# Performance work log

Hardware: AMD Instinct MI355X
Metric: run time of the kernel (lower is better)

Reference implementation:

```python
import jax, jax.numpy as jnp
import numpy as np

B, T, D, H = 8, 512, 1024, 16
DH = D // H  # per-head feature dim (64)


def setup_inputs() -> dict:
    key = jax.random.key(0)
    ks = jax.random.split(key, 10)
    s = 1.0 / np.sqrt(DH)
    inp = {
        "X_data": jax.random.normal(ks[0], (B, T, D), dtype=jnp.float32),
        "mask": jnp.ones((B, T), dtype=jnp.int32),
        # per-head Q/K/V projections (each SelfAttention has its own d_h x d_h weights)
        "Wq": jax.random.normal(ks[1], (H, DH, DH), dtype=jnp.float32) * s,
        "bq": jnp.zeros((H, DH), dtype=jnp.float32),
        "Wk": jax.random.normal(ks[2], (H, DH, DH), dtype=jnp.float32) * s,
        "bk": jnp.zeros((H, DH), dtype=jnp.float32),
        "Wv": jax.random.normal(ks[3], (H, DH, DH), dtype=jnp.float32) * s,
        "bv": jnp.zeros((H, DH), dtype=jnp.float32),
        # AttentionFusion: linear on concatenated head outputs -> len_feature_new
        "Wf": jax.random.normal(ks[4], (D, D), dtype=jnp.float32) * (1.0 / np.sqrt(D)),
        "bf": jnp.zeros((D,), dtype=jnp.float32),
    }
    return inp


def reference(X_data, mask, Wq, bq, Wk, bk, Wv, bv, Wf, bf):
    # Split features into heads: [B, T, H, DH] (equal partitions since D % H == 0)
    Xh = X_data.reshape(B, T, H, DH)
    # Batched per-head projections (replaces the Python loop over heads)
    Q = jnp.einsum("bthd,hde->bhte", Xh, Wq) + bq[None, :, None, :]
    K = jnp.einsum("bthd,hde->bhte", Xh, Wk) + bk[None, :, None, :]
    V = jnp.einsum("bthd,hde->bhte", Xh, Wv) + bv[None, :, None, :]
    scale = 1.0 / jnp.sqrt(jnp.asarray(DH, dtype=Q.dtype))
    scores = jnp.einsum("bhqe,bhke->bhqk", Q, K) * scale  # [B, H, T, T]
    scores = jnp.where(mask[:, None, None, :] > 0, scores, jnp.asarray(-1e9, scores.dtype))
    att = jax.nn.softmax(scores, axis=-1)
    out = jnp.einsum("bhqk,bhke->bhqe", att, V)  # [B, H, T, DH]
    # Concatenate heads (same order as the per-head loop) and fuse
    out = out.transpose(0, 2, 1, 3).reshape(B, T, D)
    fused = out @ Wf + bf  # AttentionFusion linear
    return fused
```

## Files before the change

kernel.cpp:

```cpp
#include <hip/hip_runtime.h>
#include <math.h>

#define B 8
#define T 512
#define D 1024
#define H 16
#define DH 64

typedef __bf16 bf16;
typedef __attribute__((ext_vector_type(8))) __bf16 bf16x8;
typedef __attribute__((ext_vector_type(4))) __bf16 bf16x4;
typedef __attribute__((ext_vector_type(4))) float f32x4;

__device__ __forceinline__ void gld16(const void* g, void* l) {
    __builtin_amdgcn_global_load_lds(
        (const __attribute__((address_space(1))) void*)g,
        (__attribute__((address_space(3))) void*)l, 16, 0, 0);
}


#define EXP2SCALE 1.44269504088896f

__global__ __launch_bounds__(256, 2) void qkv_attn(
    const float* __restrict__ X, const int* __restrict__ mask,
    const float* __restrict__ Wq, const float* __restrict__ Wk,
    const float* __restrict__ Wv,
    const float* __restrict__ bq, const float* __restrict__ bv,
    const float* __restrict__ Wf, bf16* __restrict__ WfT,
    bf16* __restrict__ Ob)
{
    __shared__ __align__(16) char smem[80384];

    if (blockIdx.x >= 512) {
        bf16* Ts = (bf16*)smem;
        const int ti = blockIdx.x - 512, tid = threadIdx.x;
        const int k0 = (ti >> 4) * 64, n0 = (ti & 15) * 64;
        for (int i = tid; i < 1024; i += 256) {
            const int k = i >> 4, nq = (i & 15) * 4;
            const float4 w = *(const float4*)(Wf + (size_t)(k0 + k) * D + n0 + nq);
            Ts[(nq + 0) * 72 + k] = (bf16)w.x; Ts[(nq + 1) * 72 + k] = (bf16)w.y;
            Ts[(nq + 2) * 72 + k] = (bf16)w.z; Ts[(nq + 3) * 72 + k] = (bf16)w.w;
        }
        __syncthreads();
        for (int i = tid; i < 512; i += 256) {
            const int n = i >> 3, kc = (i & 7) * 8;
            *(bf16x8*)(WfT + (size_t)(n0 + n) * D + k0 + kc) = *(const bf16x8*)&Ts[n * 72 + kc];
        }
        return;
    }

    bf16* Wks = (bf16*)(smem);
    bf16* Wvs = (bf16*)(smem + 8192);
    bf16* Pl  = (bf16*)(smem + 53248);
    bf16* Xkt = (bf16*)(smem + 71680);
    int*  msk = (int*)(smem + 79872);
    bf16* Wqs   = (bf16*)(smem + 16384);
    bf16* Xq    = Pl;
    bf16* Stage = Pl;
    bf16* Ostage = Pl;

    const int bh = blockIdx.x & 127, q0 = (blockIdx.x >> 7) * 128;
    const int b = bh >> 4, h = bh & 15;
    const int tid = threadIdx.x, wave = tid >> 6, lane = tid & 63;
    const int quad = lane >> 4, l15 = lane & 15;

    const int pkrow = wave * 16 + (lane >> 2);
    const int pc0 = (lane & 3) * 2;

    float bqr[4], bvr[4];
#pragma unroll
    for (int nt = 0; nt < 4; ++nt) {
        bqr[nt] = bq[h * DH + nt * 16 + l15];
        bvr[nt] = bv[h * DH + nt * 16 + l15];
    }

    float4 px0, px1, px2, px3;
    {
        const float* src = X + (size_t)(b * T + pkrow) * D + h * DH + pc0 * 8;
        px0 = *(const float4*)src; px1 = *(const float4*)(src + 4);
        px2 = *(const float4*)(src + 8); px3 = *(const float4*)(src + 12);
    }
    int mreg = (tid < 64) ? mask[(size_t)b * T + tid] : 0;

    for (int i = tid; i < 1024; i += 256) {
        const int d = i >> 4, eq4 = (i & 15) * 4;
        const int cw = ((d >> 3)) * 8 + (d & 7);
        const float4 wq4 = *(const float4*)(Wq + (size_t)h * 4096 + d * 64 + eq4);
        const float4 wk4 = *(const float4*)(Wk + (size_t)h * 4096 + d * 64 + eq4);
        const float4 wv4 = *(const float4*)(Wv + (size_t)h * 4096 + d * 64 + eq4);
#pragma unroll
        for (int j = 0; j < 4; ++j) {
            const int e = eq4 + j;
            const int idx = e * 64 + (((d >> 3) ^ (e & 7)) * 8) + (d & 7);
            Wqs[idx] = (bf16)((const float*)&wq4)[j];
            Wks[idx] = (bf16)((const float*)&wk4)[j];
            Wvs[idx] = (bf16)((const float*)&wv4)[j];
        }
        (void)cw;
    }
    for (int i = tid; i < 1024; i += 256) {
        const int row = i >> 3, c = i & 7;
        const float* src = X + (size_t)(b * T + q0 + row) * D + h * DH + c * 8;
        const float4 x0 = *(const float4*)src;
        const float4 x1 = *(const float4*)(src + 4);
        bf16x8 t;
        t[0] = (bf16)x0.x; t[1] = (bf16)x0.y; t[2] = (bf16)x0.z; t[3] = (bf16)x0.w;
        t[4] = (bf16)x1.x; t[5] = (bf16)x1.y; t[6] = (bf16)x1.z; t[7] = (bf16)x1.w;
        *(bf16x8*)&Xq[row * 64 + ((c ^ (row & 7)) * 8)] = t;
    }
    __syncthreads();

    {
        f32x4 accQ[2][4] = {};
#pragma unroll
        for (int ks = 0; ks < 2; ++ks) {
            bf16x8 af[2], bfr[4];
#pragma unroll
            for (int mt = 0; mt < 2; ++mt) {
                const int row = wave * 32 + mt * 16 + l15;
                af[mt] = *(const bf16x8*)&Xq[row * 64 + (((ks * 4 + quad) ^ (l15 & 7)) * 8)];
            }
#pragma unroll
            for (int nt = 0; nt < 4; ++nt)
                bfr[nt] = *(const bf16x8*)&Wqs[(nt * 16 + l15) * 64 + (((ks * 4 + quad) ^ (l15 & 7)) * 8)];
#pragma unroll
            for (int mt = 0; mt < 2; ++mt)
#pragma unroll
                for (int nt = 0; nt < 4; ++nt)
                    accQ[mt][nt] = __builtin_amdgcn_mfma_f32_16x16x32_bf16(af[mt], bfr[nt], accQ[mt][nt], 0, 0, 0);
        }
        __syncthreads();
        const float qs = 0.125f * EXP2SCALE;
#pragma unroll
        for (int mt = 0; mt < 2; ++mt)
#pragma unroll
            for (int nt = 0; nt < 4; ++nt)
#pragma unroll
                for (int reg = 0; reg < 4; ++reg)
                    Stage[(wave * 32 + mt * 16 + quad * 4 + reg) * 72 + nt * 16 + l15] =
                        (bf16)((accQ[mt][nt][reg] + bqr[nt]) * qs);
        __builtin_amdgcn_wave_barrier();
    }
    bf16x8 qf[2][2];
#pragma unroll
    for (int mt = 0; mt < 2; ++mt)
#pragma unroll
        for (int ks = 0; ks < 2; ++ks)
            qf[mt][ks] = *(const bf16x8*)&Stage[(wave * 32 + mt * 16 + l15) * 72 + ks * 32 + quad * 8];

    f32x4 acc[2][4] = {};
    float lst2[2] = {0.f, 0.f};

    for (int kt = 0; kt < 8; ++kt) {
        const int p = kt & 1;
        bf16* Ks  = (bf16*)(smem + 16384 + p * 9216);
        bf16* Vts = (bf16*)(smem + 34816 + p * 9216);

        {
            bf16x8 t0, t1;
            t0[0] = (bf16)px0.x; t0[1] = (bf16)px0.y; t0[2] = (bf16)px0.z; t0[3] = (bf16)px0.w;
            t0[4] = (bf16)px1.x; t0[5] = (bf16)px1.y; t0[6] = (bf16)px1.z; t0[7] = (bf16)px1.w;
            t1[0] = (bf16)px2.x; t1[1] = (bf16)px2.y; t1[2] = (bf16)px2.z; t1[3] = (bf16)px2.w;
            t1[4] = (bf16)px3.x; t1[5] = (bf16)px3.y; t1[6] = (bf16)px3.z; t1[7] = (bf16)px3.w;
            *(bf16x8*)&Xkt[pkrow * 64 + ((pc0 ^ (pkrow & 7)) * 8)] = t0;
            *(bf16x8*)&Xkt[pkrow * 64 + (((pc0 + 1) ^ (pkrow & 7)) * 8)] = t1;
            if (tid < 64) msk[p * 64 + tid] = mreg;
        }
        __builtin_amdgcn_wave_barrier();

        if (kt < 7) {
            const float* src = X + (size_t)(b * T + (kt + 1) * 64 + pkrow) * D + h * DH + pc0 * 8;
            px0 = *(const float4*)src; px1 = *(const float4*)(src + 4);
            px2 = *(const float4*)(src + 8); px3 = *(const float4*)(src + 12);
            if (tid < 64) mreg = mask[(size_t)b * T + (kt + 1) * 64 + tid];
        }

        {
            bf16x8 afkv[2];
#pragma unroll
            for (int ks = 0; ks < 2; ++ks)
                afkv[ks] = *(const bf16x8*)&Xkt[(wave * 16 + l15) * 64 + (((ks * 4 + quad) ^ (l15 & 7)) * 8)];
            f32x4 accK[4] = {}, accV[4] = {};
#pragma unroll
            for (int ks = 0; ks < 2; ++ks)
#pragma unroll
                for (int nt = 0; nt < 4; ++nt) {
                    const bf16x8 bk8 = *(const bf16x8*)&Wks[(nt * 16 + l15) * 64 + (((ks * 4 + quad) ^ (l15 & 7)) * 8)];
                    accK[nt] = __builtin_amdgcn_mfma_f32_16x16x32_bf16(bk8, afkv[ks], accK[nt], 0, 0, 0);
                    const bf16x8 bv8 = *(const bf16x8*)&Wvs[(nt * 16 + l15) * 64 + (((ks * 4 + quad) ^ (l15 & 7)) * 8)];
                    accV[nt] = __builtin_amdgcn_mfma_f32_16x16x32_bf16(afkv[ks], bv8, accV[nt], 0, 0, 0);
                }
#pragma unroll
            for (int nt = 0; nt < 4; ++nt) {
                bf16x4 kp;
#pragma unroll
                for (int reg = 0; reg < 4; ++reg) kp[reg] = (bf16)accK[nt][reg];
                *(bf16x4*)&Ks[(wave * 16 + l15) * 72 + nt * 16 + quad * 4] = kp;
                bf16x4 vp;
#pragma unroll
                for (int reg = 0; reg < 4; ++reg) vp[reg] = (bf16)accV[nt][reg];
                *(bf16x4*)&Vts[(nt * 16 + l15) * 72 + wave * 16 + quad * 4] = vp;
            }
        }
        __syncthreads();

        bf16* Plw = Pl + wave * (32 * 72);
        {
            bf16x8 kf[4][2];
#pragma unroll
            for (int nt = 0; nt < 4; ++nt)
#pragma unroll
                for (int ks = 0; ks < 2; ++ks)
                    kf[nt][ks] = *(const bf16x8*)&Ks[(nt * 16 + l15) * 72 + ks * 32 + quad * 8];
            int4 mv4[4];
#pragma unroll
            for (int nt = 0; nt < 4; ++nt)
                mv4[nt] = *(const int4*)&msk[p * 64 + nt * 16 + quad * 4];
#pragma unroll
            for (int mt = 0; mt < 2; ++mt) {
                f32x4 s[4] = {};
#pragma unroll
                for (int ks = 0; ks < 2; ++ks)
#pragma unroll
                    for (int nt = 0; nt < 4; ++nt)
                        s[nt] = __builtin_amdgcn_mfma_f32_16x16x32_bf16(kf[nt][ks], qf[mt][ks], s[nt], 0, 0, 0);
#pragma unroll
                for (int nt = 0; nt < 4; ++nt) {
                    bf16x4 pp;
                    const float p0 = (mv4[nt].x > 0) ? exp2f(s[nt][0]) : 0.f;
                    const float p1 = (mv4[nt].y > 0) ? exp2f(s[nt][1]) : 0.f;
                    const float p2 = (mv4[nt].z > 0) ? exp2f(s[nt][2]) : 0.f;
                    const float p3 = (mv4[nt].w > 0) ? exp2f(s[nt][3]) : 0.f;
                    lst2[mt] += (p0 + p1) + (p2 + p3);
                    pp[0] = (bf16)p0; pp[1] = (bf16)p1; pp[2] = (bf16)p2; pp[3] = (bf16)p3;
                    *(bf16x4*)&Plw[(mt * 16 + l15) * 72 + nt * 16 + quad * 4] = pp;
                }
            }
        }
        __builtin_amdgcn_wave_barrier();

#pragma unroll
        for (int kc = 0; kc < 2; ++kc) {
            const bf16x8 pf0 = *(const bf16x8*)&Plw[(l15) * 72 + kc * 32 + quad * 8];
            const bf16x8 pf1 = *(const bf16x8*)&Plw[(16 + l15) * 72 + kc * 32 + quad * 8];
#pragma unroll
            for (int nt = 0; nt < 4; ++nt) {
                const bf16x8 vf = *(const bf16x8*)&Vts[(nt * 16 + l15) * 72 + kc * 32 + quad * 8];
                acc[0][nt] = __builtin_amdgcn_mfma_f32_16x16x32_bf16(pf0, vf, acc[0][nt], 0, 0, 0);
                acc[1][nt] = __builtin_amdgcn_mfma_f32_16x16x32_bf16(pf1, vf, acc[1][nt], 0, 0, 0);
            }
        }
    }

    __builtin_amdgcn_wave_barrier();
    float inv_r[2][4];
#pragma unroll
    for (int mt = 0; mt < 2; ++mt) {
        float l = lst2[mt];
        l += __shfl_xor(l, 16);
        l += __shfl_xor(l, 32);
        const float inv = 1.f / l;
#pragma unroll
        for (int reg = 0; reg < 4; ++reg)
            inv_r[mt][reg] = __shfl(inv, (lane & 48) | (quad * 4 + reg));
    }
#pragma unroll
    for (int mt = 0; mt < 2; ++mt)
#pragma unroll
        for (int reg = 0; reg < 4; ++reg) {
            const int row = wave * 32 + mt * 16 + quad * 4 + reg;
#pragma unroll
            for (int nt = 0; nt < 4; ++nt)
                Ostage[row * 72 + nt * 16 + l15] =
                    (bf16)(acc[mt][nt][reg] * inv_r[mt][reg] + bvr[nt]);
        }
    __syncthreads();
    for (int i = tid; i < 1024; i += 256) {
        const int row = i >> 3, c = (i & 7) * 8;
        *(bf16x8*)(Ob + ((size_t)b * T + q0 + row) * D + h * DH + c) =
            *(const bf16x8*)&Ostage[row * 72 + c];
    }
}

__global__ __launch_bounds__(256, 2) void fuse_mfma(
    const bf16* __restrict__ Ob, const bf16* __restrict__ WfT,
    const float* __restrict__ bfv, float* __restrict__ out)
{
    __shared__ __align__(16) char smem[65536];

    const int col0 = blockIdx.x * 128;
    const int row0 = blockIdx.y * 128;
    const int tid = threadIdx.x, wave = tid >> 6, lane = tid & 63;
    const int quad = lane >> 4, l15 = lane & 15;
    const int lr = lane >> 3, lc = lane & 7;
    const int wm = wave * 32;

    f32x4 acc[2][8] = {};

    auto stage = [&](int k0, int buf) {
        bf16* As = (bf16*)(smem + buf * 16384);
        bf16* Bs = (bf16*)(smem + 32768 + buf * 16384);
#pragma unroll
        for (int j = 0; j < 4; ++j) {
            const int row = wm + j * 8 + lr;
            gld16(Ob + (size_t)(row0 + row) * D + k0 + ((lc ^ (row & 7)) * 8),
                  &As[(wm + j * 8) * 64]);
            gld16(WfT + (size_t)(col0 + row) * D + k0 + ((lc ^ (row & 7)) * 8),
                  &Bs[(wm + j * 8) * 64]);
        }
    };

    stage(0, 0);
    __syncthreads();

    for (int i = 0; i < 16; ++i) {
        const int buf = i & 1;
        if (i < 15) stage((i + 1) * 64, buf ^ 1);
        bf16* As = (bf16*)(smem + buf * 16384);
        bf16* Bs = (bf16*)(smem + 32768 + buf * 16384);
#pragma unroll
        for (int ks = 0; ks < 2; ++ks) {
            bf16x8 af[2], bfr[8];
#pragma unroll
            for (int mt = 0; mt < 2; ++mt) {
                const int row = wm + mt * 16 + l15;
                af[mt] = *(const bf16x8*)&As[row * 64 + (((ks * 4 + quad) ^ (l15 & 7)) * 8)];
            }
#pragma unroll
            for (int nt = 0; nt < 8; ++nt)
                bfr[nt] = *(const bf16x8*)&Bs[(nt * 16 + l15) * 64 + (((ks * 4 + quad) ^ (l15 & 7)) * 8)];
#pragma unroll
            for (int mt = 0; mt < 2; ++mt)
#pragma unroll
                for (int nt = 0; nt < 8; ++nt)
                    acc[mt][nt] = __builtin_amdgcn_mfma_f32_16x16x32_bf16(af[mt], bfr[nt], acc[mt][nt], 0, 0, 0);
        }
        __syncthreads();
    }

    float* Ofs = (float*)smem;
    float bias[8];
#pragma unroll
    for (int nt = 0; nt < 8; ++nt) bias[nt] = bfv[col0 + nt * 16 + l15];
#pragma unroll
    for (int cp = 0; cp < 2; ++cp) {
        if (cp) __syncthreads();
#pragma unroll
        for (int mt = 0; mt < 2; ++mt)
#pragma unroll
            for (int reg = 0; reg < 4; ++reg) {
                const int row = wm + mt * 16 + quad * 4 + reg;
#pragma unroll
                for (int nn = 0; nn < 4; ++nn)
                    Ofs[row * 68 + nn * 16 + l15] = acc[mt][cp * 4 + nn][reg] + bias[cp * 4 + nn];
            }
        __syncthreads();
        for (int i = tid; i < 2048; i += 256) {
            const int row = i >> 4, c = (i & 15) * 4;
            *(float4*)(out + (size_t)(row0 + row) * D + col0 + cp * 64 + c) =
                *(const float4*)&Ofs[row * 68 + c];
        }
    }
}

extern "C" void kernel_launch(void* const* d_in, const int* in_sizes, int n_in,
                              void* d_out, int out_size, void* d_ws, size_t ws_size,
                              hipStream_t stream) {
    const float* X   = (const float*)d_in[0];
    const int* mask  = (const int*)d_in[1];
    const float* Wq  = (const float*)d_in[2];
    const float* bq  = (const float*)d_in[3];
    const float* Wk  = (const float*)d_in[4];
    const float* bk  = (const float*)d_in[5];
    const float* Wv  = (const float*)d_in[6];
    const float* bv  = (const float*)d_in[7];
    const float* Wf  = (const float*)d_in[8];
    const float* bfv = (const float*)d_in[9];
    float* out = (float*)d_out;
    (void)bk;

    bf16* wsb = (bf16*)d_ws;
    const size_t QN = (size_t)B * H * T * DH;
    bf16* Ob  = wsb;
    bf16* WfT = wsb + QN;

    qkv_attn<<<dim3(768), 256, 0, stream>>>(X, mask, Wq, Wk, Wv, bq, bv, Wf, WfT, Ob);
    fuse_mfma<<<dim3(D / 128, (B * T) / 128), 256, 0, stream>>>(Ob, WfT, bfv, out);
}
```

Measured before the change: 126.0 us.

## Fuse attention and output projection into one kernel with flag-based inter-block sync

```diff
diff --git a/kernel.cpp b/kernel.cpp
--- a/kernel.cpp
+++ b/kernel.cpp
@@ -20,33 +20,43 @@
 
 
 #define EXP2SCALE 1.44269504088896f
-
-__global__ __launch_bounds__(256, 2) void qkv_attn(
+#define MAGIC 0x5AD0C0DEu
+
+__global__ __launch_bounds__(256, 2) void fused_all(
     const float* __restrict__ X, const int* __restrict__ mask,
     const float* __restrict__ Wq, const float* __restrict__ Wk,
     const float* __restrict__ Wv,
     const float* __restrict__ bq, const float* __restrict__ bv,
     const float* __restrict__ Wf, bf16* __restrict__ WfT,
-    bf16* __restrict__ Ob)
+    bf16* __restrict__ Ob,
+    unsigned int* __restrict__ obF, unsigned int* __restrict__ wfF,
+    const float* __restrict__ bfv, float* __restrict__ out)
 {
     __shared__ __align__(16) char smem[80384];
 
-    if (blockIdx.x >= 512) {
+    const int bid = blockIdx.x, tid = threadIdx.x;
+    const int wave = tid >> 6, lane = tid & 63;
+    const int quad = lane >> 4, l15 = lane & 15;
+    const int lr = lane >> 3, lc = lane & 7;
+
+    {
         bf16* Ts = (bf16*)smem;
-        const int ti = blockIdx.x - 512, tid = threadIdx.x;
-        const int k0 = (ti >> 4) * 64, n0 = (ti & 15) * 64;
-        for (int i = tid; i < 1024; i += 256) {
-            const int k = i >> 4, nq = (i & 15) * 4;
+        const int tj = bid >> 1, half = bid & 1;
+        const int k0 = (tj >> 4) * 64, n0 = (tj & 15) * 64 + half * 32;
+        for (int i = tid; i < 512; i += 256) {
+            const int k = i >> 3, nq = (i & 7) * 4;
             const float4 w = *(const float4*)(Wf + (size_t)(k0 + k) * D + n0 + nq);
             Ts[(nq + 0) * 72 + k] = (bf16)w.x; Ts[(nq + 1) * 72 + k] = (bf16)w.y;
             Ts[(nq + 2) * 72 + k] = (bf16)w.z; Ts[(nq + 3) * 72 + k] = (bf16)w.w;
         }
         __syncthreads();
-        for (int i = tid; i < 512; i += 256) {
+        for (int i = tid; i < 256; i += 256) {
             const int n = i >> 3, kc = (i & 7) * 8;
             *(bf16x8*)(WfT + (size_t)(n0 + n) * D + k0 + kc) = *(const bf16x8*)&Ts[n * 72 + kc];
         }
-        return;
+        __syncthreads();
+        if (tid == 0)
+            __hip_atomic_store(&wfF[bid], MAGIC, __ATOMIC_RELEASE, __HIP_MEMORY_SCOPE_AGENT);
     }
 
     bf16* Wks = (bf16*)(smem);
@@ -59,10 +69,8 @@
     bf16* Stage = Pl;
     bf16* Ostage = Pl;
 
-    const int bh = blockIdx.x & 127, q0 = (blockIdx.x >> 7) * 128;
+    const int bh = bid & 127, q0 = (bid >> 7) * 128;
     const int b = bh >> 4, h = bh & 15;
-    const int tid = threadIdx.x, wave = tid >> 6, lane = tid & 63;
-    const int quad = lane >> 4, l15 = lane & 15;
 
     const int pkrow = wave * 16 + (lane >> 2);
     const int pc0 = (lane & 3) * 2;
@@ -84,7 +92,6 @@
 
     for (int i = tid; i < 1024; i += 256) {
         const int d = i >> 4, eq4 = (i & 15) * 4;
-        const int cw = ((d >> 3)) * 8 + (d & 7);
         const float4 wq4 = *(const float4*)(Wq + (size_t)h * 4096 + d * 64 + eq4);
         const float4 wk4 = *(const float4*)(Wk + (size_t)h * 4096 + d * 64 + eq4);
         const float4 wv4 = *(const float4*)(Wv + (size_t)h * 4096 + d * 64 + eq4);
@@ -96,7 +103,6 @@
             Wks[idx] = (bf16)((const float*)&wk4)[j];
             Wvs[idx] = (bf16)((const float*)&wv4)[j];
         }
-        (void)cw;
     }
     for (int i = tid; i < 1024; i += 256) {
         const int row = i >> 3, c = i & 7;
@@ -280,85 +286,93 @@
         *(bf16x8*)(Ob + ((size_t)b * T + q0 + row) * D + h * DH + c) =
             *(const bf16x8*)&Ostage[row * 72 + c];
     }
-}
-
-__global__ __launch_bounds__(256, 2) void fuse_mfma(
-    const bf16* __restrict__ Ob, const bf16* __restrict__ WfT,
-    const float* __restrict__ bfv, float* __restrict__ out)
-{
-    __shared__ __align__(16) char smem[65536];
-
-    const int col0 = blockIdx.x * 128;
-    const int row0 = blockIdx.y * 128;
-    const int tid = threadIdx.x, wave = tid >> 6, lane = tid & 63;
-    const int quad = lane >> 4, l15 = lane & 15;
-    const int lr = lane >> 3, lc = lane & 7;
-    const int wm = wave * 32;
-
-    f32x4 acc[2][8] = {};
-
-    auto stage = [&](int k0, int buf) {
-        bf16* As = (bf16*)(smem + buf * 16384);
-        bf16* Bs = (bf16*)(smem + 32768 + buf * 16384);
-#pragma unroll
-        for (int j = 0; j < 4; ++j) {
-            const int row = wm + j * 8 + lr;
-            gld16(Ob + (size_t)(row0 + row) * D + k0 + ((lc ^ (row & 7)) * 8),
-                  &As[(wm + j * 8) * 64]);
-            gld16(WfT + (size_t)(col0 + row) * D + k0 + ((lc ^ (row & 7)) * 8),
-                  &Bs[(wm + j * 8) * 64]);
-        }
-    };
-
-    stage(0, 0);
     __syncthreads();
-
-    for (int i = 0; i < 16; ++i) {
-        const int buf = i & 1;
-        if (i < 15) stage((i + 1) * 64, buf ^ 1);
-        bf16* As = (bf16*)(smem + buf * 16384);
-        bf16* Bs = (bf16*)(smem + 32768 + buf * 16384);
-#pragma unroll
-        for (int ks = 0; ks < 2; ++ks) {
-            bf16x8 af[2], bfr[8];
-#pragma unroll
-            for (int mt = 0; mt < 2; ++mt) {
-                const int row = wm + mt * 16 + l15;
-                af[mt] = *(const bf16x8*)&As[row * 64 + (((ks * 4 + quad) ^ (l15 & 7)) * 8)];
-            }
-#pragma unroll
-            for (int nt = 0; nt < 8; ++nt)
-                bfr[nt] = *(const bf16x8*)&Bs[(nt * 16 + l15) * 64 + (((ks * 4 + quad) ^ (l15 & 7)) * 8)];
-#pragma unroll
-            for (int mt = 0; mt < 2; ++mt)
-#pragma unroll
-                for (int nt = 0; nt < 8; ++nt)
-                    acc[mt][nt] = __builtin_amdgcn_mfma_f32_16x16x32_bf16(af[mt], bfr[nt], acc[mt][nt], 0, 0, 0);
-        }
-        __syncthreads();
-    }
-
-    float* Ofs = (float*)smem;
-    float bias[8];
-#pragma unroll
-    for (int nt = 0; nt < 8; ++nt) bias[nt] = bfv[col0 + nt * 16 + l15];
-#pragma unroll
-    for (int cp = 0; cp < 2; ++cp) {
-        if (cp) __syncthreads();
+    if (tid == 0)
+        __hip_atomic_store(&obF[bid], MAGIC, __ATOMIC_RELEASE, __HIP_MEMORY_SCOPE_AGENT);
+
+    const int rb = bid >> 4, cb = bid & 15;
+    {
+        const int b2 = rb >> 2, qc2 = rb & 3;
+        if (tid < 16) {
+            const unsigned int* f = &obF[qc2 * 128 + b2 * 16 + tid];
+            while (__hip_atomic_load(f, __ATOMIC_ACQUIRE, __HIP_MEMORY_SCOPE_AGENT) != MAGIC)
+                __builtin_amdgcn_s_sleep(2);
+        } else if (tid < 48) {
+            const int j = tid - 16;
+            const unsigned int* f = &wfF[32 * (j >> 1) + 2 * cb + (j & 1)];
+            while (__hip_atomic_load(f, __ATOMIC_ACQUIRE, __HIP_MEMORY_SCOPE_AGENT) != MAGIC)
+                __builtin_amdgcn_s_sleep(2);
+        }
+        __syncthreads();
+    }
+
+    {
+        const int col0 = cb * 64, row0 = rb * 128;
+        const int wm = wave * 32;
+        f32x4 facc[2][4] = {};
+
+        auto stage = [&](int k0, int buf) {
+            bf16* As = (bf16*)(smem + buf * 16384);
+            bf16* Bs = (bf16*)(smem + 32768 + buf * 8192);
+#pragma unroll
+            for (int j = 0; j < 4; ++j) {
+                const int row = wm + j * 8 + lr;
+                gld16(Ob + (size_t)(row0 + row) * D + k0 + ((lc ^ (row & 7)) * 8),
+                      &As[(wm + j * 8) * 64]);
+            }
+#pragma unroll
+            for (int j = 0; j < 2; ++j) {
+                const int row = wave * 16 + j * 8 + lr;
+                gld16(WfT + (size_t)(col0 + row) * D + k0 + ((lc ^ (row & 7)) * 8),
+                      &Bs[(wave * 16 + j * 8) * 64]);
+            }
+        };
+
+        stage(0, 0);
+        __syncthreads();
+
+        for (int i = 0; i < 16; ++i) {
+            const int buf = i & 1;
+            if (i < 15) stage((i + 1) * 64, buf ^ 1);
+            bf16* As = (bf16*)(smem + buf * 16384);
+            bf16* Bs = (bf16*)(smem + 32768 + buf * 8192);
+#pragma unroll
+            for (int ks = 0; ks < 2; ++ks) {
+                bf16x8 af[2], bfr[4];
+#pragma unroll
+                for (int mt = 0; mt < 2; ++mt) {
+                    const int row = wm + mt * 16 + l15;
+                    af[mt] = *(const bf16x8*)&As[row * 64 + (((ks * 4 + quad) ^ (l15 & 7)) * 8)];
+                }
+#pragma unroll
+                for (int nt = 0; nt < 4; ++nt)
+                    bfr[nt] = *(const bf16x8*)&Bs[(nt * 16 + l15) * 64 + (((ks * 4 + quad) ^ (l15 & 7)) * 8)];
+#pragma unroll
+                for (int mt = 0; mt < 2; ++mt)
+#pragma unroll
+                    for (int nt = 0; nt < 4; ++nt)
+                        facc[mt][nt] = __builtin_amdgcn_mfma_f32_16x16x32_bf16(af[mt], bfr[nt], facc[mt][nt], 0, 0, 0);
+            }
+            __syncthreads();
+        }
+
+        float* Ofs = (float*)smem;
+        float bias[4];
+#pragma unroll
+        for (int nt = 0; nt < 4; ++nt) bias[nt] = bfv[col0 + nt * 16 + l15];
 #pragma unroll
         for (int mt = 0; mt < 2; ++mt)
 #pragma unroll
             for (int reg = 0; reg < 4; ++reg) {
                 const int row = wm + mt * 16 + quad * 4 + reg;
 #pragma unroll
-                for (int nn = 0; nn < 4; ++nn)
-                    Ofs[row * 68 + nn * 16 + l15] = acc[mt][cp * 4 + nn][reg] + bias[cp * 4 + nn];
+                for (int nt = 0; nt < 4; ++nt)
+                    Ofs[row * 68 + nt * 16 + l15] = facc[mt][nt][reg] + bias[nt];
             }
         __syncthreads();
         for (int i = tid; i < 2048; i += 256) {
             const int row = i >> 4, c = (i & 15) * 4;
-            *(float4*)(out + (size_t)(row0 + row) * D + col0 + cp * 64 + c) =
-                *(const float4*)&Ofs[row * 68 + c];
+            *(float4*)(out + (size_t)(row0 + row) * D + col0 + c) = *(const float4*)&Ofs[row * 68 + c];
         }
     }
 }
@@ -383,7 +397,9 @@
     const size_t QN = (size_t)B * H * T * DH;
     bf16* Ob  = wsb;
     bf16* WfT = wsb + QN;
-
-    qkv_attn<<<dim3(768), 256, 0, stream>>>(X, mask, Wq, Wk, Wv, bq, bv, Wf, WfT, Ob);
-    fuse_mfma<<<dim3(D / 128, (B * T) / 128), 256, 0, stream>>>(Ob, WfT, bfv, out);
+    unsigned int* obF = (unsigned int*)(wsb + QN + (size_t)D * D);
+    unsigned int* wfF = obF + 512;
+
+    fused_all<<<dim3(512), 256, 0, stream>>>(X, mask, Wq, Wk, Wv, bq, bv,
+                                             Wf, WfT, Ob, obF, wfF, bfv, out);
 }
```

New measurement: 153.6 us. 21.9% more time.

## Double block size to 512 threads and split attention work across 8 waves

Applied to the files above, without the earlier changes.

```diff
diff --git a/kernel.cpp b/kernel.cpp
--- a/kernel.cpp
+++ b/kernel.cpp
@@ -21,7 +21,7 @@
 
 #define EXP2SCALE 1.44269504088896f
 
-__global__ __launch_bounds__(256, 2) void qkv_attn(
+__global__ __launch_bounds__(512, 4) void qkv_attn(
     const float* __restrict__ X, const int* __restrict__ mask,
     const float* __restrict__ Wq, const float* __restrict__ Wk,
     const float* __restrict__ Wv,
@@ -29,20 +29,21 @@
     const float* __restrict__ Wf, bf16* __restrict__ WfT,
     bf16* __restrict__ Ob)
 {
-    __shared__ __align__(16) char smem[80384];
-
-    if (blockIdx.x >= 512) {
+    __shared__ __align__(16) char smem[71680];
+    const int bid = blockIdx.x, tid = threadIdx.x;
+
+    if (bid >= 512) {
         bf16* Ts = (bf16*)smem;
-        const int ti = blockIdx.x - 512, tid = threadIdx.x;
+        const int ti = bid - 512;
         const int k0 = (ti >> 4) * 64, n0 = (ti & 15) * 64;
-        for (int i = tid; i < 1024; i += 256) {
+        for (int i = tid; i < 1024; i += 512) {
             const int k = i >> 4, nq = (i & 15) * 4;
             const float4 w = *(const float4*)(Wf + (size_t)(k0 + k) * D + n0 + nq);
             Ts[(nq + 0) * 72 + k] = (bf16)w.x; Ts[(nq + 1) * 72 + k] = (bf16)w.y;
             Ts[(nq + 2) * 72 + k] = (bf16)w.z; Ts[(nq + 3) * 72 + k] = (bf16)w.w;
         }
         __syncthreads();
-        for (int i = tid; i < 512; i += 256) {
+        for (int i = tid; i < 512; i += 512) {
             const int n = i >> 3, kc = (i & 7) * 8;
             *(bf16x8*)(WfT + (size_t)(n0 + n) * D + k0 + kc) = *(const bf16x8*)&Ts[n * 72 + kc];
         }
@@ -52,20 +53,16 @@
     bf16* Wks = (bf16*)(smem);
     bf16* Wvs = (bf16*)(smem + 8192);
     bf16* Pl  = (bf16*)(smem + 53248);
-    bf16* Xkt = (bf16*)(smem + 71680);
-    int*  msk = (int*)(smem + 79872);
-    bf16* Wqs   = (bf16*)(smem + 16384);
-    bf16* Xq    = Pl;
+    bf16* Wqs = (bf16*)(smem + 16384);
+    bf16* Xq  = Pl;
     bf16* Stage = Pl;
     bf16* Ostage = Pl;
 
-    const int bh = blockIdx.x & 127, q0 = (blockIdx.x >> 7) * 128;
+    const int bh = bid & 127, q0 = (bid >> 7) * 128;
     const int b = bh >> 4, h = bh & 15;
-    const int tid = threadIdx.x, wave = tid >> 6, lane = tid & 63;
+    const int wave = tid >> 6, lane = tid & 63;
     const int quad = lane >> 4, l15 = lane & 15;
-
-    const int pkrow = wave * 16 + (lane >> 2);
-    const int pc0 = (lane & 3) * 2;
+    const int wv = wave & 3;
 
     float bqr[4], bvr[4];
 #pragma unroll
@@ -74,17 +71,31 @@
         bvr[nt] = bv[h * DH + nt * 16 + l15];
     }
 
+    auto mbits = [&](int kt) -> unsigned {
+        unsigned m = 0;
+#pragma unroll
+        for (int nt = 0; nt < 4; ++nt) {
+            const int4 v = *(const int4*)&mask[(size_t)b * T + kt * 64 + nt * 16 + quad * 4];
+            m |= (v.x > 0 ? 1u : 0u) << (nt * 4 + 0);
+            m |= (v.y > 0 ? 1u : 0u) << (nt * 4 + 1);
+            m |= (v.z > 0 ? 1u : 0u) << (nt * 4 + 2);
+            m |= (v.w > 0 ? 1u : 0u) << (nt * 4 + 3);
+        }
+        return m;
+    };
+
     float4 px0, px1, px2, px3;
     {
-        const float* src = X + (size_t)(b * T + pkrow) * D + h * DH + pc0 * 8;
-        px0 = *(const float4*)src; px1 = *(const float4*)(src + 4);
-        px2 = *(const float4*)(src + 8); px3 = *(const float4*)(src + 12);
-    }
-    int mreg = (tid < 64) ? mask[(size_t)b * T + tid] : 0;
-
-    for (int i = tid; i < 1024; i += 256) {
+        const float* src = X + (size_t)(b * T + wv * 16 + l15) * D + h * DH;
+        px0 = *(const float4*)(src + quad * 8);
+        px1 = *(const float4*)(src + quad * 8 + 4);
+        px2 = *(const float4*)(src + 32 + quad * 8);
+        px3 = *(const float4*)(src + 32 + quad * 8 + 4);
+    }
+    unsigned mcur = mbits(0), mnxt = 0;
+
+    for (int i = tid; i < 1024; i += 512) {
         const int d = i >> 4, eq4 = (i & 15) * 4;
-        const int cw = ((d >> 3)) * 8 + (d & 7);
         const float4 wq4 = *(const float4*)(Wq + (size_t)h * 4096 + d * 64 + eq4);
         const float4 wk4 = *(const float4*)(Wk + (size_t)h * 4096 + d * 64 + eq4);
         const float4 wv4 = *(const float4*)(Wv + (size_t)h * 4096 + d * 64 + eq4);
@@ -96,9 +107,8 @@
             Wks[idx] = (bf16)((const float*)&wk4)[j];
             Wvs[idx] = (bf16)((const float*)&wv4)[j];
         }
-        (void)cw;
-    }
-    for (int i = tid; i < 1024; i += 256) {
+    }
+    for (int i = tid; i < 1024; i += 512) {
         const int row = i >> 3, c = i & 7;
         const float* src = X + (size_t)(b * T + q0 + row) * D + h * DH + c * 8;
         const float4 x0 = *(const float4*)src;
@@ -111,202 +121,182 @@
     __syncthreads();
 
     {
-        f32x4 accQ[2][4] = {};
+        f32x4 accQ[4] = {};
 #pragma unroll
         for (int ks = 0; ks < 2; ++ks) {
-            bf16x8 af[2], bfr[4];
-#pragma unroll
-            for (int mt = 0; mt < 2; ++mt) {
-                const int row = wave * 32 + mt * 16 + l15;
-                af[mt] = *(const bf16x8*)&Xq[row * 64 + (((ks * 4 + quad) ^ (l15 & 7)) * 8)];
+            const bf16x8 a8 = *(const bf16x8*)&Xq[(wave * 16 + l15) * 64 + (((ks * 4 + quad) ^ (l15 & 7)) * 8)];
+#pragma unroll
+            for (int nt = 0; nt < 4; ++nt) {
+                const bf16x8 w8 = *(const bf16x8*)&Wqs[(nt * 16 + l15) * 64 + (((ks * 4 + quad) ^ (l15 & 7)) * 8)];
+                accQ[nt] = __builtin_amdgcn_mfma_f32_16x16x32_bf16(a8, w8, accQ[nt], 0, 0, 0);
             }
-#pragma unroll
-            for (int nt = 0; nt < 4; ++nt)
-                bfr[nt] = *(const bf16x8*)&Wqs[(nt * 16 + l15) * 64 + (((ks * 4 + quad) ^ (l15 & 7)) * 8)];
-#pragma unroll
-            for (int mt = 0; mt < 2; ++mt)
-#pragma unroll
-                for (int nt = 0; nt < 4; ++nt)
-                    accQ[mt][nt] = __builtin_amdgcn_mfma_f32_16x16x32_bf16(af[mt], bfr[nt], accQ[mt][nt], 0, 0, 0);
         }
         __syncthreads();
         const float qs = 0.125f * EXP2SCALE;
 #pragma unroll
-        for (int mt = 0; mt < 2; ++mt)
-#pragma unroll
-            for (int nt = 0; nt < 4; ++nt)
-#pragma unroll
-                for (int reg = 0; reg < 4; ++reg)
-                    Stage[(wave * 32 + mt * 16 + quad * 4 + reg) * 72 + nt * 16 + l15] =
-                        (bf16)((accQ[mt][nt][reg] + bqr[nt]) * qs);
+        for (int nt = 0; nt < 4; ++nt)
+#pragma unroll
+            for (int reg = 0; reg < 4; ++reg)
+                Stage[(wave * 16 + quad * 4 + reg) * 72 + nt * 16 + l15] =
+                    (bf16)((accQ[nt][reg] + bqr[nt]) * qs);
         __builtin_amdgcn_wave_barrier();
     }
-    bf16x8 qf[2][2];
-#pragma unroll
-    for (int mt = 0; mt < 2; ++mt)
-#pragma unroll
-        for (int ks = 0; ks < 2; ++ks)
-            qf[mt][ks] = *(const bf16x8*)&Stage[(wave * 32 + mt * 16 + l15) * 72 + ks * 32 + quad * 8];
-
-    f32x4 acc[2][4] = {};
-    float lst2[2] = {0.f, 0.f};
+    bf16x8 qf[2];
+#pragma unroll
+    for (int ks = 0; ks < 2; ++ks)
+        qf[ks] = *(const bf16x8*)&Stage[(wave * 16 + l15) * 72 + ks * 32 + quad * 8];
+    __builtin_amdgcn_wave_barrier();
+
+    f32x4 acc[4] = {};
+    float lsum = 0.f;
+    bf16* Plw = Pl + wave * (16 * 72);
 
     for (int kt = 0; kt < 8; ++kt) {
         const int p = kt & 1;
         bf16* Ks  = (bf16*)(smem + 16384 + p * 9216);
         bf16* Vts = (bf16*)(smem + 34816 + p * 9216);
 
+        bf16x8 af0, af1;
+        af0[0] = (bf16)px0.x; af0[1] = (bf16)px0.y; af0[2] = (bf16)px0.z; af0[3] = (bf16)px0.w;
+        af0[4] = (bf16)px1.x; af0[5] = (bf16)px1.y; af0[6] = (bf16)px1.z; af0[7] = (bf16)px1.w;
+        af1[0] = (bf16)px2.x; af1[1] = (bf16)px2.y; af1[2] = (bf16)px2.z; af1[3] = (bf16)px2.w;
+        af1[4] = (bf16)px3.x; af1[5] = (bf16)px3.y; af1[6] = (bf16)px3.z; af1[7] = (bf16)px3.w;
+
+        if (kt < 7) {
+            const float* src = X + (size_t)(b * T + (kt + 1) * 64 + wv * 16 + l15) * D + h * DH;
+            px0 = *(const float4*)(src + quad * 8);
+            px1 = *(const float4*)(src + quad * 8 + 4);
+            px2 = *(const float4*)(src + 32 + quad * 8);
+            px3 = *(const float4*)(src + 32 + quad * 8 + 4);
+            mnxt = mbits(kt + 1);
+        }
+
         {
-            bf16x8 t0, t1;
-            t0[0] = (bf16)px0.x; t0[1] = (bf16)px0.y; t0[2] = (bf16)px0.z; t0[3] = (bf16)px0.w;
-            t0[4] = (bf16)px1.x; t0[5] = (bf16)px1.y; t0[6] = (bf16)px1.z; t0[7] = (bf16)px1.w;
-            t1[0] = (bf16)px2.x; t1[1] = (bf16)px2.y; t1[2] = (bf16)px2.z; t1[3] = (bf16)px2.w;
-            t1[4] = (bf16)px3.x; t1[5] = (bf16)px3.y; t1[6] = (bf16)px3.z; t1[7] = (bf16)px3.w;
-            *(bf16x8*)&Xkt[pkrow * 64 + ((pc0 ^ (pkrow & 7)) * 8)] = t0;
-            *(bf16x8*)&Xkt[pkrow * 64 + (((pc0 + 1) ^ (pkrow & 7)) * 8)] = t1;
-            if (tid < 64) msk[p * 64 + tid] = mreg;
+            f32x4 akv[4] = {};
+            if (wave < 4) {
+#pragma unroll
+                for (int ks = 0; ks < 2; ++ks) {
+                    const bf16x8 a8 = (ks == 0) ? af0 : af1;
+#pragma unroll
+                    for (int nt = 0; nt < 4; ++nt) {
+                        const bf16x8 w8 = *(const bf16x8*)&Wks[(nt * 16 + l15) * 64 + (((ks * 4 + quad) ^ (l15 & 7)) * 8)];
+                        akv[nt] = __builtin_amdgcn_mfma_f32_16x16x32_bf16(w8, a8, akv[nt], 0, 0, 0);
+                    }
+                }
+#pragma unroll
+                for (int nt = 0; nt < 4; ++nt) {
+                    bf16x4 kp;
+#pragma unroll
+                    for (int reg = 0; reg < 4; ++reg) kp[reg] = (bf16)akv[nt][reg];
+                    *(bf16x4*)&Ks[(wv * 16 + l15) * 72 + nt * 16 + quad * 4] = kp;
+                }
+            } else {
+#pragma unroll
+                for (int ks = 0; ks < 2; ++ks) {
+                    const bf16x8 a8 = (ks == 0) ? af0 : af1;
+#pragma unroll
+                    for (int nt = 0; nt < 4; ++nt) {
+                        const bf16x8 w8 = *(const bf16x8*)&Wvs[(nt * 16 + l15) * 64 + (((ks * 4 + quad) ^ (l15 & 7)) * 8)];
+                        akv[nt] = __builtin_amdgcn_mfma_f32_16x16x32_bf16(a8, w8, akv[nt], 0, 0, 0);
+                    }
+                }
+#pragma unroll
+                for (int nt = 0; nt < 4; ++nt) {
+                    bf16x4 vp;
+#pragma unroll
+                    for (int reg = 0; reg < 4; ++reg) vp[reg] = (bf16)akv[nt][reg];
+                    *(bf16x4*)&Vts[(nt * 16 + l15) * 72 + wv * 16 + quad * 4] = vp;
+                }
+            }
+        }
+        __syncthreads();
+
+        {
+            f32x4 s[4] = {};
+#pragma unroll
+            for (int ks = 0; ks < 2; ++ks)
+#pragma unroll
+                for (int nt = 0; nt < 4; ++nt) {
+                    const bf16x8 k8 = *(const bf16x8*)&Ks[(nt * 16 + l15) * 72 + ks * 32 + quad * 8];
+                    s[nt] = __builtin_amdgcn_mfma_f32_16x16x32_bf16(k8, qf[ks], s[nt], 0, 0, 0);
+                }
+#pragma unroll
+            for (int nt = 0; nt < 4; ++nt) {
+                const float p0 = ((mcur >> (nt * 4 + 0)) & 1) ? exp2f(s[nt][0]) : 0.f;
+                const float p1 = ((mcur >> (nt * 4 + 1)) & 1) ? exp2f(s[nt][1]) : 0.f;
+                const float p2 = ((mcur >> (nt * 4 + 2)) & 1) ? exp2f(s[nt][2]) : 0.f;
+                const float p3 = ((mcur >> (nt * 4 + 3)) & 1) ? exp2f(s[nt][3]) : 0.f;
+                lsum += (p0 + p1) + (p2 + p3);
+                bf16x4 pp;
+                pp[0] = (bf16)p0; pp[1] = (bf16)p1; pp[2] = (bf16)p2; pp[3] = (bf16)p3;
+                *(bf16x4*)&Plw[l15 * 72 + nt * 16 + quad * 4] = pp;
+            }
         }
         __builtin_amdgcn_wave_barrier();
 
-        if (kt < 7) {
-            const float* src = X + (size_t)(b * T + (kt + 1) * 64 + pkrow) * D + h * DH + pc0 * 8;
-            px0 = *(const float4*)src; px1 = *(const float4*)(src + 4);
-            px2 = *(const float4*)(src + 8); px3 = *(const float4*)(src + 12);
-            if (tid < 64) mreg = mask[(size_t)b * T + (kt + 1) * 64 + tid];
-        }
-
-        {
-            bf16x8 afkv[2];
-#pragma unroll
-            for (int ks = 0; ks < 2; ++ks)
-                afkv[ks] = *(const bf16x8*)&Xkt[(wave * 16 + l15) * 64 + (((ks * 4 + quad) ^ (l15 & 7)) * 8)];
-            f32x4 accK[4] = {}, accV[4] = {};
-#pragma unroll
-            for (int ks = 0; ks < 2; ++ks)
-#pragma unroll
-                for (int nt = 0; nt < 4; ++nt) {
-                    const bf16x8 bk8 = *(const bf16x8*)&Wks[(nt * 16 + l15) * 64 + (((ks * 4 + quad) ^ (l15 & 7)) * 8)];
-                    accK[nt] = __builtin_amdgcn_mfma_f32_16x16x32_bf16(bk8, afkv[ks], accK[nt], 0, 0, 0);
-                    const bf16x8 bv8 = *(const bf16x8*)&Wvs[(nt * 16 + l15) * 64 + (((ks * 4 + quad) ^ (l15 & 7)) * 8)];
-                    accV[nt] = __builtin_amdgcn_mfma_f32_16x16x32_bf16(afkv[ks], bv8, accV[nt], 0, 0, 0);
-                }
-#pragma unroll
-            for (int nt = 0; nt < 4; ++nt) {
-                bf16x4 kp;
-#pragma unroll
-                for (int reg = 0; reg < 4; ++reg) kp[reg] = (bf16)accK[nt][reg];
-                *(bf16x4*)&Ks[(wave * 16 + l15) * 72 + nt * 16 + quad * 4] = kp;
-                bf16x4 vp;
-#pragma unroll
-                for (int reg = 0; reg < 4; ++reg) vp[reg] = (bf16)accV[nt][reg];
-                *(bf16x4*)&Vts[(nt * 16 + l15) * 72 + wave * 16 + quad * 4] = vp;
-            }
-        }
-        __syncthreads();
-
-        bf16* Plw = Pl + wave * (32 * 72);
-        {
-            bf16x8 kf[4][2];
-#pragma unroll
-            for (int nt = 0; nt < 4; ++nt)
-#pragma unroll
-                for (int ks = 0; ks < 2; ++ks)
-                    kf[nt][ks] = *(const bf16x8*)&Ks[(nt * 16 + l15) * 72 + ks * 32 + quad * 8];
-            int4 mv4[4];
-#pragma unroll
-            for (int nt = 0; nt < 4; ++nt)
-                mv4[nt] = *(const int4*)&msk[p * 64 + nt * 16 + quad * 4];
-#pragma unroll
-            for (int mt = 0; mt < 2; ++mt) {
-                f32x4 s[4] = {};
-#pragma unroll
-                for (int ks = 0; ks < 2; ++ks)
-#pragma unroll
-                    for (int nt = 0; nt < 4; ++nt)
-                        s[nt] = __builtin_amdgcn_mfma_f32_16x16x32_bf16(kf[nt][ks], qf[mt][ks], s[nt], 0, 0, 0);
-#pragma unroll
-                for (int nt = 0; nt < 4; ++nt) {
-                    bf16x4 pp;
-                    const float p0 = (mv4[nt].x > 0) ? exp2f(s[nt][0]) : 0.f;
-                    const float p1 = (mv4[nt].y > 0) ? exp2f(s[nt][1]) : 0.f;
-                    const float p2 = (mv4[nt].z > 0) ? exp2f(s[nt][2]) : 0.f;
-                    const float p3 = (mv4[nt].w > 0) ? exp2f(s[nt][3]) : 0.f;
-                    lst2[mt] += (p0 + p1) + (p2 + p3);
-                    pp[0] = (bf16)p0; pp[1] = (bf16)p1; pp[2] = (bf16)p2; pp[3] = (bf16)p3;
-                    *(bf16x4*)&Plw[(mt * 16 + l15) * 72 + nt * 16 + quad * 4] = pp;
-                }
-            }
-        }
-        __builtin_amdgcn_wave_barrier();
-
 #pragma unroll
         for (int kc = 0; kc < 2; ++kc) {
-            const bf16x8 pf0 = *(const bf16x8*)&Plw[(l15) * 72 + kc * 32 + quad * 8];
-            const bf16x8 pf1 = *(const bf16x8*)&Plw[(16 + l15) * 72 + kc * 32 + quad * 8];
+            const bf16x8 pf = *(const bf16x8*)&Plw[l15 * 72 + kc * 32 + quad * 8];
 #pragma unroll
             for (int nt = 0; nt < 4; ++nt) {
                 const bf16x8 vf = *(const bf16x8*)&Vts[(nt * 16 + l15) * 72 + kc * 32 + quad * 8];
-                acc[0][nt] = __builtin_amdgcn_mfma_f32_16x16x32_bf16(pf0, vf, acc[0][nt], 0, 0, 0);
-                acc[1][nt] = __builtin_amdgcn_mfma_f32_16x16x32_bf16(pf1, vf, acc[1][nt], 0, 0, 0);
+                acc[nt] = __builtin_amdgcn_mfma_f32_16x16x32_bf16(pf, vf, acc[nt], 0, 0, 0);
             }
         }
+        mcur = mnxt;
     }
 
     __builtin_amdgcn_wave_barrier();
-    float inv_r[2][4];
-#pragma unroll
-    for (int mt = 0; mt < 2; ++mt) {
-        float l = lst2[mt];
-        l += __shfl_xor(l, 16);
-        l += __shfl_xor(l, 32);
-        const float inv = 1.f / l;
+    float l = lsum;
+    l += __shfl_xor(l, 16);
+    l += __shfl_xor(l, 32);
+    const float inv = 1.f / l;
+    float inv_r[4];
+#pragma unroll
+    for (int reg = 0; reg < 4; ++reg)
+        inv_r[reg] = __shfl(inv, (lane & 48) | (quad * 4 + reg));
+#pragma unroll
+    for (int nt = 0; nt < 4; ++nt)
 #pragma unroll
         for (int reg = 0; reg < 4; ++reg)
-            inv_r[mt][reg] = __shfl(inv, (lane & 48) | (quad * 4 + reg));
-    }
-#pragma unroll
-    for (int mt = 0; mt < 2; ++mt)
-#pragma unroll
-        for (int reg = 0; reg < 4; ++reg) {
-            const int row = wave * 32 + mt * 16 + quad * 4 + reg;
-#pragma unroll
-            for (int nt = 0; nt < 4; ++nt)
-                Ostage[row * 72 + nt * 16 + l15] =
-                    (bf16)(acc[mt][nt][reg] * inv_r[mt][reg] + bvr[nt]);
-        }
+            Ostage[(wave * 16 + quad * 4 + reg) * 72 + nt * 16 + l15] =
+                (bf16)(acc[nt][reg] * inv_r[reg] + bvr[nt]);
     __syncthreads();
-    for (int i = tid; i < 1024; i += 256) {
+    for (int i = tid; i < 1024; i += 512) {
         const int row = i >> 3, c = (i & 7) * 8;
         *(bf16x8*)(Ob + ((size_t)b * T + q0 + row) * D + h * DH + c) =
             *(const bf16x8*)&Ostage[row * 72 + c];
     }
 }
 
-__global__ __launch_bounds__(256, 2) void fuse_mfma(
+__global__ __launch_bounds__(512, 4) void fuse_mfma(
     const bf16* __restrict__ Ob, const bf16* __restrict__ WfT,
     const float* __restrict__ bfv, float* __restrict__ out)
 {
-    __shared__ __align__(16) char smem[65536];
-
-    const int col0 = blockIdx.x * 128;
+    __shared__ __align__(16) char smem[49152];
+
+    const int col0 = blockIdx.x * 64;
     const int row0 = blockIdx.y * 128;
     const int tid = threadIdx.x, wave = tid >> 6, lane = tid & 63;
     const int quad = lane >> 4, l15 = lane & 15;
     const int lr = lane >> 3, lc = lane & 7;
-    const int wm = wave * 32;
-
-    f32x4 acc[2][8] = {};
+    const int wm = (wave >> 1) * 32, wn = (wave & 1) * 32;
+
+    f32x4 acc[2][2] = {};
 
     auto stage = [&](int k0, int buf) {
         bf16* As = (bf16*)(smem + buf * 16384);
-        bf16* Bs = (bf16*)(smem + 32768 + buf * 16384);
-#pragma unroll
-        for (int j = 0; j < 4; ++j) {
-            const int row = wm + j * 8 + lr;
+        bf16* Bs = (bf16*)(smem + 32768 + buf * 8192);
+#pragma unroll
+        for (int j = 0; j < 2; ++j) {
+            const int row = wave * 16 + j * 8 + lr;
             gld16(Ob + (size_t)(row0 + row) * D + k0 + ((lc ^ (row & 7)) * 8),
-                  &As[(wm + j * 8) * 64]);
+                  &As[(wave * 16 + j * 8) * 64]);
+        }
+        {
+            const int row = wave * 8 + lr;
             gld16(WfT + (size_t)(col0 + row) * D + k0 + ((lc ^ (row & 7)) * 8),
-                  &Bs[(wm + j * 8) * 64]);
+                  &Bs[(wave * 8) * 64]);
         }
     };
 
@@ -317,49 +307,42 @@
         const int buf = i & 1;
         if (i < 15) stage((i + 1) * 64, buf ^ 1);
         bf16* As = (bf16*)(smem + buf * 16384);
-        bf16* Bs = (bf16*)(smem + 32768 + buf * 16384);
+        bf16* Bs = (bf16*)(smem + 32768 + buf * 8192);
 #pragma unroll
         for (int ks = 0; ks < 2; ++ks) {
-            bf16x8 af[2], bfr[8];
-#pragma unroll
-            for (int mt = 0; mt < 2; ++mt) {
-                const int row = wm + mt * 16 + l15;
-                af[mt] = *(const bf16x8*)&As[row * 64 + (((ks * 4 + quad) ^ (l15 & 7)) * 8)];
-            }
-#pragma unroll
-            for (int nt = 0; nt < 8; ++nt)
-                bfr[nt] = *(const bf16x8*)&Bs[(nt * 16 + l15) * 64 + (((ks * 4 + quad) ^ (l15 & 7)) * 8)];
+            bf16x8 af[2], bfr[2];
 #pragma unroll
             for (int mt = 0; mt < 2; ++mt)
-#pragma unroll
-                for (int nt = 0; nt < 8; ++nt)
+                af[mt] = *(const bf16x8*)&As[(wm + mt * 16 + l15) * 64 + (((ks * 4 + quad) ^ (l15 & 7)) * 8)];
+#pragma unroll
+            for (int nt = 0; nt < 2; ++nt)
+                bfr[nt] = *(const bf16x8*)&Bs[(wn + nt * 16 + l15) * 64 + (((ks * 4 + quad) ^ (l15 & 7)) * 8)];
+#pragma unroll
+            for (int mt = 0; mt < 2; ++mt)
+#pragma unroll
+                for (int nt = 0; nt < 2; ++nt)
                     acc[mt][nt] = __builtin_amdgcn_mfma_f32_16x16x32_bf16(af[mt], bfr[nt], acc[mt][nt], 0, 0, 0);
         }
         __syncthreads();
     }
 
     float* Ofs = (float*)smem;
-    float bias[8];
-#pragma unroll
-    for (int nt = 0; nt < 8; ++nt) bias[nt] = bfv[col0 + nt * 16 + l15];
-#pragma unroll
-    for (int cp = 0; cp < 2; ++cp) {
-        if (cp) __syncthreads();
-#pragma unroll
-        for (int mt = 0; mt < 2; ++mt)
-#pragma unroll
-            for (int reg = 0; reg < 4; ++reg) {
-                const int row = wm + mt * 16 + quad * 4 + reg;
-#pragma unroll
-                for (int nn = 0; nn < 4; ++nn)
-                    Ofs[row * 68 + nn * 16 + l15] = acc[mt][cp * 4 + nn][reg] + bias[cp * 4 + nn];
-            }
-        __syncthreads();
-        for (int i = tid; i < 2048; i += 256) {
-            const int row = i >> 4, c = (i & 15) * 4;
-            *(float4*)(out + (size_t)(row0 + row) * D + col0 + cp * 64 + c) =
-                *(const float4*)&Ofs[row * 68 + c];
-        }
+    float bias[2];
+#pragma unroll
+    for (int nt = 0; nt < 2; ++nt) bias[nt] = bfv[col0 + wn + nt * 16 + l15];
+#pragma unroll
+    for (int mt = 0; mt < 2; ++mt)
+#pragma unroll
+        for (int reg = 0; reg < 4; ++reg) {
+            const int row = wm + mt * 16 + quad * 4 + reg;
+#pragma unroll
+            for (int nt = 0; nt < 2; ++nt)
+                Ofs[row * 68 + wn + nt * 16 + l15] = acc[mt][nt][reg] + bias[nt];
+        }
+    __syncthreads();
+    for (int i = tid; i < 2048; i += 512) {
+        const int row = i >> 4, c = (i & 15) * 4;
+        *(float4*)(out + (size_t)(row0 + row) * D + col0 + c) = *(const float4*)&Ofs[row * 68 + c];
     }
 }
 
@@ -384,6 +367,6 @@
     bf16* Ob  = wsb;
     bf16* WfT = wsb + QN;
 
-    qkv_attn<<<dim3(768), 256, 0, stream>>>(X, mask, Wq, Wk, Wv, bq, bv, Wf, WfT, Ob);
-    fuse_mfma<<<dim3(D / 128, (B * T) / 128), 256, 0, stream>>>(Ob, WfT, bfv, out);
+    qkv_attn<<<dim3(768), 512, 0, stream>>>(X, mask, Wq, Wk, Wv, bq, bv, Wf, WfT, Ob);
+    fuse_mfma<<<dim3(D / 64, (B * T) / 128), 512, 0, stream>>>(Ob, WfT, bfv, out);
 }
```

After: 129.3 us. 2.6% more time.

## Retile fusion GEMM to 128x64 blocks with triple-buffered async LDS pipeline

Applied to the files above, without the earlier changes.

```diff
diff --git a/kernel.cpp b/kernel.cpp
--- a/kernel.cpp
+++ b/kernel.cpp
@@ -84,7 +84,6 @@
 
     for (int i = tid; i < 1024; i += 256) {
         const int d = i >> 4, eq4 = (i & 15) * 4;
-        const int cw = ((d >> 3)) * 8 + (d & 7);
         const float4 wq4 = *(const float4*)(Wq + (size_t)h * 4096 + d * 64 + eq4);
         const float4 wk4 = *(const float4*)(Wk + (size_t)h * 4096 + d * 64 + eq4);
         const float4 wv4 = *(const float4*)(Wv + (size_t)h * 4096 + d * 64 + eq4);
@@ -96,7 +95,6 @@
             Wks[idx] = (bf16)((const float*)&wk4)[j];
             Wvs[idx] = (bf16)((const float*)&wv4)[j];
         }
-        (void)cw;
     }
     for (int i = tid; i < 1024; i += 256) {
         const int row = i >> 3, c = i & 7;
@@ -282,84 +280,84 @@
     }
 }
 
-__global__ __launch_bounds__(256, 2) void fuse_mfma(
+__global__ __launch_bounds__(512, 4) void fuse_mfma(
     const bf16* __restrict__ Ob, const bf16* __restrict__ WfT,
     const float* __restrict__ bfv, float* __restrict__ out)
 {
-    __shared__ __align__(16) char smem[65536];
-
-    const int col0 = blockIdx.x * 128;
+    __shared__ __align__(16) char smem[73728];
+
+    const int col0 = blockIdx.x * 64;
     const int row0 = blockIdx.y * 128;
     const int tid = threadIdx.x, wave = tid >> 6, lane = tid & 63;
     const int quad = lane >> 4, l15 = lane & 15;
     const int lr = lane >> 3, lc = lane & 7;
-    const int wm = wave * 32;
-
-    f32x4 acc[2][8] = {};
-
-    auto stage = [&](int k0, int buf) {
-        bf16* As = (bf16*)(smem + buf * 16384);
-        bf16* Bs = (bf16*)(smem + 32768 + buf * 16384);
-#pragma unroll
-        for (int j = 0; j < 4; ++j) {
-            const int row = wm + j * 8 + lr;
+    const int wm = (wave >> 1) * 32, wn = (wave & 1) * 32;
+
+    f32x4 acc[2][2] = {};
+
+    auto stage = [&](int t) {
+        const int buf = t - (t / 3) * 3;
+        bf16* As = (bf16*)(smem + buf * 24576);
+        bf16* Bs = (bf16*)(smem + buf * 24576 + 16384);
+        const int k0 = t * 64;
+#pragma unroll
+        for (int j = 0; j < 2; ++j) {
+            const int row = wave * 16 + j * 8 + lr;
             gld16(Ob + (size_t)(row0 + row) * D + k0 + ((lc ^ (row & 7)) * 8),
-                  &As[(wm + j * 8) * 64]);
-            gld16(WfT + (size_t)(col0 + row) * D + k0 + ((lc ^ (row & 7)) * 8),
-                  &Bs[(wm + j * 8) * 64]);
-        }
+                  &As[(wave * 16 + j * 8) * 64]);
+        }
+        const int rowB = wave * 8 + lr;
+        gld16(WfT + (size_t)(col0 + rowB) * D + k0 + ((lc ^ (rowB & 7)) * 8),
+              &Bs[(wave * 8) * 64]);
     };
 
-    stage(0, 0);
+    stage(0);
+    stage(1);
+
+    for (int i = 0; i < 16; ++i) {
+        if (i < 15) asm volatile("s_waitcnt vmcnt(3)" ::: "memory");
+        else        asm volatile("s_waitcnt vmcnt(0)" ::: "memory");
+        __builtin_amdgcn_s_barrier();
+
+        const int buf = i - (i / 3) * 3;
+        bf16* As = (bf16*)(smem + buf * 24576);
+        bf16* Bs = (bf16*)(smem + buf * 24576 + 16384);
+#pragma unroll
+        for (int ks = 0; ks < 2; ++ks) {
+            bf16x8 af[2], bfr[2];
+#pragma unroll
+            for (int mt = 0; mt < 2; ++mt)
+                af[mt] = *(const bf16x8*)&As[(wm + mt * 16 + l15) * 64 + (((ks * 4 + quad) ^ (l15 & 7)) * 8)];
+#pragma unroll
+            for (int nt = 0; nt < 2; ++nt)
+                bfr[nt] = *(const bf16x8*)&Bs[(wn + nt * 16 + l15) * 64 + (((ks * 4 + quad) ^ (l15 & 7)) * 8)];
+#pragma unroll
+            for (int mt = 0; mt < 2; ++mt)
+#pragma unroll
+                for (int nt = 0; nt < 2; ++nt)
+                    acc[mt][nt] = __builtin_amdgcn_mfma_f32_16x16x32_bf16(af[mt], bfr[nt], acc[mt][nt], 0, 0, 0);
+        }
+        if (i < 14) stage(i + 2);
+    }
     __syncthreads();
 
-    for (int i = 0; i < 16; ++i) {
-        const int buf = i & 1;
-        if (i < 15) stage((i + 1) * 64, buf ^ 1);
-        bf16* As = (bf16*)(smem + buf * 16384);
-        bf16* Bs = (bf16*)(smem + 32768 + buf * 16384);
-#pragma unroll
-        for (int ks = 0; ks < 2; ++ks) {
-            bf16x8 af[2], bfr[8];
-#pragma unroll
-            for (int mt = 0; mt < 2; ++mt) {
-                const int row = wm + mt * 16 + l15;
-                af[mt] = *(const bf16x8*)&As[row * 64 + (((ks * 4 + quad) ^ (l15 & 7)) * 8)];
-            }
-#pragma unroll
-            for (int nt = 0; nt < 8; ++nt)
-                bfr[nt] = *(const bf16x8*)&Bs[(nt * 16 + l15) * 64 + (((ks * 4 + quad) ^ (l15 & 7)) * 8)];
-#pragma unroll
-            for (int mt = 0; mt < 2; ++mt)
-#pragma unroll
-                for (int nt = 0; nt < 8; ++nt)
-                    acc[mt][nt] = __builtin_amdgcn_mfma_f32_16x16x32_bf16(af[mt], bfr[nt], acc[mt][nt], 0, 0, 0);
-        }
-        __syncthreads();
-    }
-
     float* Ofs = (float*)smem;
-    float bias[8];
-#pragma unroll
-    for (int nt = 0; nt < 8; ++nt) bias[nt] = bfv[col0 + nt * 16 + l15];
-#pragma unroll
-    for (int cp = 0; cp < 2; ++cp) {
-        if (cp) __syncthreads();
-#pragma unroll
-        for (int mt = 0; mt < 2; ++mt)
-#pragma unroll
-            for (int reg = 0; reg < 4; ++reg) {
-                const int row = wm + mt * 16 + quad * 4 + reg;
-#pragma unroll
-                for (int nn = 0; nn < 4; ++nn)
-                    Ofs[row * 68 + nn * 16 + l15] = acc[mt][cp * 4 + nn][reg] + bias[cp * 4 + nn];
-            }
-        __syncthreads();
-        for (int i = tid; i < 2048; i += 256) {
-            const int row = i >> 4, c = (i & 15) * 4;
-            *(float4*)(out + (size_t)(row0 + row) * D + col0 + cp * 64 + c) =
-                *(const float4*)&Ofs[row * 68 + c];
-        }
+    float bias[2];
+#pragma unroll
+    for (int nt = 0; nt < 2; ++nt) bias[nt] = bfv[col0 + wn + nt * 16 + l15];
+#pragma unroll
+    for (int mt = 0; mt < 2; ++mt)
+#pragma unroll
+        for (int reg = 0; reg < 4; ++reg) {
+            const int row = wm + mt * 16 + quad * 4 + reg;
+#pragma unroll
+            for (int nt = 0; nt < 2; ++nt)
+                Ofs[row * 68 + wn + nt * 16 + l15] = acc[mt][nt][reg] + bias[nt];
+        }
+    __syncthreads();
+    for (int i = tid; i < 2048; i += 512) {
+        const int row = i >> 4, c = (i & 15) * 4;
+        *(float4*)(out + (size_t)(row0 + row) * D + col0 + c) = *(const float4*)&Ofs[row * 68 + c];
     }
 }
 
@@ -385,5 +383,5 @@
     bf16* WfT = wsb + QN;
 
     qkv_attn<<<dim3(768), 256, 0, stream>>>(X, mask, Wq, Wk, Wv, bq, bv, Wf, WfT, Ob);
-    fuse_mfma<<<dim3(D / 128, (B * T) / 128), 256, 0, stream>>>(Ob, WfT, bfv, out);
+    fuse_mfma<<<dim3(D / 64, (B * T) / 128), 512, 0, stream>>>(Ob, WfT, bfv, out);
 }
```

After: 125.7 us. About the same (-0.2%).
